# Kernel tuning notes

Hardware: AMD Instinct MI355X
Metric: run time of the kernel (lower is better)

Reference implementation:

```python
import jax, jax.numpy as jnp
import numpy as np

H, W, C = 2160, 3840, 3
K = 1  # kernel_size (splat radius window)


def setup_inputs() -> dict:
    key = jax.random.key(0)
    k1, k2, k3 = jax.random.split(key, 3)
    img = jax.random.normal(k1, (H, W, C), dtype=jnp.float32)
    flow = jax.random.normal(k2, (1, H, W, 2), dtype=jnp.float32) * 4.0  # dx, dy
    depth = jax.random.uniform(k3, (H, W), dtype=jnp.float32, minval=0.1, maxval=10.0)
    return {"img": img, "flow": flow, "depth": depth}


def reference(img, flow, depth):
    """Forward flow-based splatting with per-pixel depth z-buffer test.

    Each source pixel (y,x) is splatted to round((x,y) + flow) within a
    K x K kernel window; where multiple sources land on the same target
    pixel, the one with the smallest depth wins (z-buffer).
    """
    h, w, c = img.shape
    f = flow[0]  # [h, w, 2]
    xs = jnp.arange(w, dtype=f.dtype)
    ys = jnp.arange(h, dtype=f.dtype)
    tx0 = xs[None, :] + f[..., 0]  # target x, [h, w]
    ty0 = ys[:, None] + f[..., 1]  # target y, [h, w]

    offs = [(dy, dx)
            for dy in range(-(K // 2), (K - 1) // 2 + 1)
            for dx in range(-(K // 2), (K - 1) // 2 + 1)]

    dflat = depth.reshape(-1)            # [h*w]
    img_flat = img.reshape(-1, c)        # [h*w, c]

    idx_list, dep_list, src_list = [], [], []
    for dy, dx in offs:
        tx = jnp.round(tx0 + dx).astype(jnp.int32)
        ty = jnp.round(ty0 + dy).astype(jnp.int32)
        valid = (tx >= 0) & (tx < w) & (ty >= 0) & (ty < h)
        lin = jnp.where(valid, ty * w + tx, -1).reshape(-1)  # -1 -> dropped
        idx_list.append(lin)
        dep_list.append(dflat)
        src_list.append(img_flat)

    idx = jnp.concatenate(idx_list)   # [n_splats]
    dep = jnp.concatenate(dep_list)   # [n_splats]
    src = jnp.concatenate(src_list)   # [n_splats, c]

    # Pass 1: scatter-min depth into z-buffer (out-of-bounds dropped).
    zbuf = jnp.full(h * w, jnp.inf, dtype=dep.dtype).at[idx].min(dep, mode='drop')
    # Pass 2: only the depth-test winners write their color.
    win = (dep <= zbuf[jnp.clip(idx, 0, h * w - 1)]) & (idx >= 0)
    widx = jnp.where(win, idx, -1)
    out = jnp.zeros((h * w, c), dtype=img.dtype).at[widx].add(
        src * win[:, None].astype(src.dtype), mode='drop')
    return out.reshape(h, w, c)
```

## Files before the change

kernel.cpp:

```cpp
#include <hip/hip_runtime.h>

constexpr int H = 2160, W = 3840;
constexpr int NPIX = H * W;
constexpr int M = 20;
constexpr int TW = 64, TH = 64;
constexpr int TS = TW * TH;
constexpr int WW = TW + 2 * M;
constexpr int TXN = W / TW;
constexpr int TYN = (H + TH - 1) / TH;
constexpr int NTILES = TXN * TYN;
constexpr int BLK = 1024;
constexpr int QROW = WW / 4;
constexpr int RPP = BLK / QROW;
constexpr unsigned long long EMPTY = ~0ULL;
constexpr unsigned FAR_CAP = 65536;
static_assert(WW % 4 == 0 && RPP * 3 >= TH + 2 * M, "sweep geometry");



__global__ void __launch_bounds__(256)
prep_kernel(const float4* __restrict__ flow4, const float4* __restrict__ depth4,
            uint4* __restrict__ tgt16_4,
            unsigned long long* __restrict__ overlay,
            unsigned int* __restrict__ farcount,
            unsigned int* __restrict__ dirty,
            uint4* __restrict__ farlist)
{
    int tid8 = blockIdx.x * 256 + threadIdx.x;
    unsigned long long oobkey = EMPTY;
    if (tid8 < NPIX / 8) {
        int i0 = tid8 * 8;
        int y  = i0 / W;
        int x0 = i0 - y * W;
        int q0 = tid8 * 2;
        float4 fa0 = flow4[q0 * 2];
        float4 fa1 = flow4[q0 * 2 + 1];
        float4 fb0 = flow4[q0 * 2 + 2];
        float4 fb1 = flow4[q0 * 2 + 3];
        float4 d0  = depth4[q0];
        float4 d1  = depth4[q0 + 1];
        float fx[8] = {fa0.x, fa0.z, fa1.x, fa1.z, fb0.x, fb0.z, fb1.x, fb1.z};
        float fy[8] = {fa0.y, fa0.w, fa1.y, fa1.w, fb0.y, fb0.w, fb1.y, fb1.w};
        float dz[8] = {d0.x, d0.y, d0.z, d0.w, d1.x, d1.y, d1.z, d1.w};
        unsigned short tv[8];
        #pragma unroll
        for (int c = 0; c < 8; ++c) {
            int x = x0 + c;
            int tx = (int)rintf((float)x + fx[c]);
            int ty = (int)rintf((float)y + fy[c]);
            bool valid = ((unsigned)tx < (unsigned)W) && ((unsigned)ty < (unsigned)H);
            unsigned short t = 0xFFFFu;
            if (!valid) {
                unsigned db = __float_as_uint(dz[c]);
                unsigned long long k =
                    ((unsigned long long)db << 32) | 0x80000000u | (unsigned)(i0 + c);
                oobkey = k < oobkey ? k : oobkey;
                dirty[NTILES - 1] = 1;
            } else {
                int dx = tx - x, dy = ty - y;
                bool far = ((unsigned)(dx + M) > (unsigned)(2 * M)) ||
                           ((unsigned)(dy + M) > (unsigned)(2 * M));
                if (far) {
                    unsigned db  = __float_as_uint(dz[c]);
                    int lin = ty * W + tx;
                    unsigned long long key =
                        ((unsigned long long)db << 32) | (unsigned)(i0 + c);
                    atomicMin(&overlay[lin], key);
                    dirty[(ty / TH) * TXN + (tx / TW)] = 1;
                    unsigned slot = atomicAdd(farcount, 1u);
                    if (slot < FAR_CAP)
                        farlist[slot] = make_uint4((unsigned)lin, db,
                                                   (unsigned)(i0 + c), 0u);
                } else {
                    t = (unsigned short)(((dy + M) << 6) | (dx + M));
                }
            }
            tv[c] = t;
        }
        uint4 sv;
        sv.x = (unsigned)tv[0] | ((unsigned)tv[1] << 16);
        sv.y = (unsigned)tv[2] | ((unsigned)tv[3] << 16);
        sv.z = (unsigned)tv[4] | ((unsigned)tv[5] << 16);
        sv.w = (unsigned)tv[6] | ((unsigned)tv[7] << 16);
        tgt16_4[tid8] = sv;
    }
    #pragma unroll
    for (int o = 32; o > 0; o >>= 1) {
        unsigned long long other = __shfl_down(oobkey, o);
        oobkey = other < oobkey ? other : oobkey;
    }
    if ((threadIdx.x & 63) == 0 && oobkey != EMPTY)
        atomicMin(&overlay[NPIX - 1], oobkey);
}

__global__ void __launch_bounds__(BLK, 8)
resolve_kernel(const unsigned short* __restrict__ tgt16,
               const float* __restrict__ depth,
               const float* __restrict__ img,
               unsigned long long* __restrict__ overlay,
               const unsigned int* __restrict__ dirty,
               float* __restrict__ out)
{
    __shared__ unsigned long long lkey[TS];
    __shared__ int lflag;
    const int tid = threadIdx.x;
    const int tile = (blockIdx.x % 8) * (NTILES / 8) + blockIdx.x / 8;
    const int tyi = tile / TXN, txi = tile - tyi * TXN;
    const int ty0 = tyi * TH, tx0 = txi * TW;

    #pragma unroll
    for (int pp = 0; pp < TS / BLK; ++pp) lkey[pp * BLK + tid] = EMPTY;
    if (tid == 0) lflag = 0;
    __syncthreads();

    const int wy_lo = max(ty0 - M, 0);
    const int wy_hi = min(ty0 + TH + M, H);
    const int nrows = wy_hi - wy_lo;
    const int nwin  = nrows * WW;
    const int myrow = tid / QROW;
    const int myq   = tid - myrow * QROW;
    const int gxb   = tx0 - M + myq * 4;
    const bool qok  = (myrow < RPP) && ((unsigned)gxb < (unsigned)W);

    auto LOADR = [&](int pass, ushort4& t4, float4& d4) -> bool {
        int row = pass * RPP + myrow;
        bool act = qok && (row < nrows);
        int gy  = wy_lo + min(row, nrows - 1);
        int gxc = min(max(gxb, 0), W - 4);
        size_t base = (size_t)gy * W + gxc;
        t4 = *(const ushort4*)(&tgt16[base]);
        d4 = *(const float4*)(&depth[base]);
        return act;
    };
    auto PROCR = [&](int pass, bool act, ushort4 t4, float4 d4) {
        if (!act) return;
        int gy = wy_lo + pass * RPP + myrow;
        unsigned tt[4] = {t4.x, t4.y, t4.z, t4.w};
        float    dz[4] = {d4.x, d4.y, d4.z, d4.w};
        #pragma unroll
        for (int c = 0; c < 4; ++c) {
            unsigned t = tt[c];
            int gx = gxb + c;
            int tx = gx + (int)(t & 63u) - M;
            int ty = gy + (int)(t >> 6) - M;
            unsigned ltx = (unsigned)(tx - tx0);
            unsigned lty = (unsigned)(ty - ty0);
            if (ltx >= (unsigned)TW || lty >= (unsigned)TH) continue;
            unsigned p  = lty * TW + ltx;
            unsigned gi = (unsigned)(gy * W + gx);
            unsigned long long key =
                ((unsigned long long)__float_as_uint(dz[c]) << 32) | gi;
            unsigned long long old = atomicMin(&lkey[p], key);
            if ((unsigned)(old >> 32) == (unsigned)(key >> 32) && old != key)
                lflag = 1;
        }
    };

    ushort4 ta, tb; float4 da, db_;
    bool actA = LOADR(0, ta, da);
    bool actB = LOADR(1, tb, db_);
    PROCR(0, actA, ta, da);
    bool actC = LOADR(2, ta, da);
    PROCR(1, actB, tb, db_);
    PROCR(2, actC, ta, da);
    __syncthreads();

    const bool isdirty = dirty[tile] != 0;

    #pragma unroll
    for (int pp = 0; pp < TS / BLK; ++pp) {
        int p = pp * BLK + tid;
        int ly = p >> 6, lx = p & 63;
        int gy = ty0 + ly, gx = tx0 + lx;
        if (gy >= H) continue;
        int gi = gy * W + gx;
        unsigned long long k = lkey[p];
        if (isdirty) {
            unsigned long long o = overlay[gi];
            if ((o >> 32) == (k >> 32) && o != k && k != EMPTY) lflag = 1;
            if (o < k) k = o;
            lkey[p] = k;
            overlay[gi] = k;
        }
        float r = 0.f, g = 0.f, b = 0.f;
        if (k != EMPTY && !((unsigned)k & 0x80000000u)) {
            int src = (int)((unsigned)k & 0x7FFFFFFFu);
            r = img[3 * src + 0];
            g = img[3 * src + 1];
            b = img[3 * src + 2];
        }
        out[3 * gi + 0] = r;
        out[3 * gi + 1] = g;
        out[3 * gi + 2] = b;
    }
    __syncthreads();

    if (lflag) {
        const int wx_lo = tx0 - M;
        for (int j = tid; j < nwin; j += BLK) {
            int wy = j / WW;
            int wx = j - wy * WW;
            int gy = wy_lo + wy;
            int gx = wx_lo + wx;
            if ((unsigned)gx >= (unsigned)W) continue;
            int gi = gy * W + gx;
            unsigned t = tgt16[gi];
            int tx = gx + (int)(t & 63u) - M;
            int ty = gy + (int)(t >> 6) - M;
            unsigned ltx = (unsigned)(tx - tx0);
            unsigned lty = (unsigned)(ty - ty0);
            if (ltx >= (unsigned)TW || lty >= (unsigned)TH) continue;
            unsigned long long k = lkey[lty * TW + ltx];
            unsigned db = __float_as_uint(depth[gi]);
            if ((unsigned)(k >> 32) == db && ((unsigned)k & 0x7FFFFFFFu) != (unsigned)gi) {
                int lin = ty * W + tx;
                atomicAdd(&out[3 * lin + 0], img[3 * gi + 0]);
                atomicAdd(&out[3 * lin + 1], img[3 * gi + 1]);
                atomicAdd(&out[3 * lin + 2], img[3 * gi + 2]);
            }
        }
    }
}

__global__ void __launch_bounds__(256)
farfix_kernel(const uint4* __restrict__ farlist,
              const unsigned int* __restrict__ farcount,
              const unsigned long long* __restrict__ overlay,
              const float* __restrict__ img, float* __restrict__ out)
{
    unsigned n = *farcount;
    if (n > FAR_CAP) n = FAR_CAP;
    for (unsigned r = blockIdx.x * 256 + threadIdx.x; r < n; r += gridDim.x * 256) {
        uint4 rec = farlist[r];
        unsigned long long k = overlay[rec.x];
        if ((unsigned)(k >> 32) == rec.y && ((unsigned)k & 0x7FFFFFFFu) != rec.z) {
            atomicAdd(&out[3 * rec.x + 0], img[3 * rec.z + 0]);
            atomicAdd(&out[3 * rec.x + 1], img[3 * rec.z + 1]);
            atomicAdd(&out[3 * rec.x + 2], img[3 * rec.z + 2]);
        }
    }
}


__global__ void __launch_bounds__(256)
fb_zmin(const float2* __restrict__ flow, const float* __restrict__ depth,
        unsigned long long* __restrict__ zbuf)
{
    int i = blockIdx.x * 256 + threadIdx.x;
    if (i >= NPIX) return;
    int y = i / W, x = i - y * W;
    float2 f = flow[i];
    int tx = (int)rintf((float)x + f.x);
    int ty = (int)rintf((float)y + f.y);
    bool valid = (tx >= 0) && (tx < W) && (ty >= 0) && (ty < H);
    int lin = valid ? (ty * W + tx) : (NPIX - 1);
    unsigned db = __float_as_uint(depth[i]);
    unsigned long long key = ((unsigned long long)db << 32) | (unsigned)i | (valid ? 0u : 0x80000000u);
    if (zbuf[lin] > key) atomicMin(&zbuf[lin], key);
}

__global__ void __launch_bounds__(256)
fb_gather(const unsigned long long* __restrict__ zbuf,
          const float* __restrict__ img, float* __restrict__ out)
{
    int t = blockIdx.x * 256 + threadIdx.x;
    if (t >= NPIX) return;
    unsigned long long key = zbuf[t];
    float r = 0.f, g = 0.f, b = 0.f;
    if (key != EMPTY && !((unsigned)key & 0x80000000u)) {
        int src = (int)((unsigned)key & 0x7FFFFFFFu);
        r = img[3 * src + 0]; g = img[3 * src + 1]; b = img[3 * src + 2];
    }
    out[3 * t + 0] = r; out[3 * t + 1] = g; out[3 * t + 2] = b;
}

__global__ void __launch_bounds__(256)
fb_tiefix(const float2* __restrict__ flow, const float* __restrict__ depth,
          const float* __restrict__ img,
          const unsigned long long* __restrict__ zbuf, float* __restrict__ out)
{
    int i = blockIdx.x * 256 + threadIdx.x;
    if (i >= NPIX) return;
    int y = i / W, x = i - y * W;
    float2 f = flow[i];
    int tx = (int)rintf((float)x + f.x);
    int ty = (int)rintf((float)y + f.y);
    if (tx < 0 || tx >= W || ty < 0 || ty >= H) return;
    int lin = ty * W + tx;
    unsigned long long key = zbuf[lin];
    unsigned db = __float_as_uint(depth[i]);
    if (db == (unsigned)(key >> 32) && (unsigned)key != (unsigned)i) {
        atomicAdd(&out[3 * lin + 0], img[3 * i + 0]);
        atomicAdd(&out[3 * lin + 1], img[3 * i + 1]);
        atomicAdd(&out[3 * lin + 2], img[3 * i + 2]);
    }
}

extern "C" void kernel_launch(void* const* d_in, const int* in_sizes, int n_in,
                              void* d_out, int out_size, void* d_ws, size_t ws_size,
                              hipStream_t stream) {
    const float*  img   = (const float*)d_in[0];
    const float2* flow  = (const float2*)d_in[1];
    const float*  depth = (const float*)d_in[2];
    float* out = (float*)d_out;
    char* ws = (char*)d_ws;

    const size_t off_overlay = (size_t)NPIX * 2;
    const size_t off_meta    = off_overlay + (size_t)NPIX * 8;
    const size_t off_dirty   = off_meta + 16;
    const size_t off_far     = off_dirty + (size_t)NTILES * 4;
    const size_t need = off_far + (size_t)FAR_CAP * 16;

    dim3 blk(256), grd((NPIX + 255) / 256);

    if (ws_size >= need) {
        uint4*              tgt16_4  = (uint4*)ws;
        unsigned long long* overlay  = (unsigned long long*)(ws + off_overlay);
        unsigned int*       farcount = (unsigned int*)(ws + off_meta);
        unsigned int*       dirtyf   = (unsigned int*)(ws + off_dirty);
        uint4*              farlist  = (uint4*)(ws + off_far);

        hipMemsetAsync(ws + off_meta, 0, 16 + (size_t)NTILES * 4, stream);

        prep_kernel<<<dim3(NPIX / 8 / 256), blk, 0, stream>>>(
            (const float4*)flow, (const float4*)depth, tgt16_4, overlay,
            farcount, dirtyf, farlist);
        resolve_kernel<<<dim3(NTILES), dim3(BLK), 0, stream>>>(
            (const unsigned short*)ws, depth, img, overlay, dirtyf, out);
        farfix_kernel<<<dim3(64), blk, 0, stream>>>(farlist, farcount, overlay,
                                                    img, out);
    } else {
        unsigned long long* zbuf = (unsigned long long*)ws;
        hipMemsetAsync(zbuf, 0xFF, (size_t)NPIX * 8, stream);
        fb_zmin  <<<grd, blk, 0, stream>>>(flow, depth, zbuf);
        fb_gather<<<grd, blk, 0, stream>>>(zbuf, img, out);
        fb_tiefix<<<grd, blk, 0, stream>>>(flow, depth, img, zbuf, out);
    }
}
```

Measured before the change: 111.9 us.

## Fuse far-splat fixup into resolve kernel, shrink tiles, add nontemporal accesses

Removes the separate farfix kernel launch and instead has each dirty tile scan the far list and apply tie fixups for its own pixels using the shared-memory key buffer. Tiles are halved to 64x32 with 512-thread blocks and a fourth row pass. The shared-memory init now runs after the first loads are issued, the overlay writeback is dropped, and flow loads and output stores are made nontemporal. The risk is that every dirty tile rescans the whole far list, which is redundant work when that list is large, and the smaller tiles add halo overhead.

```diff
diff --git a/kernel.cpp b/kernel.cpp
--- a/kernel.cpp
+++ b/kernel.cpp
@@ -3,23 +3,25 @@
 constexpr int H = 2160, W = 3840;
 constexpr int NPIX = H * W;
 constexpr int M = 20;
-constexpr int TW = 64, TH = 64;
+constexpr int TW = 64, TH = 32;
 constexpr int TS = TW * TH;
 constexpr int WW = TW + 2 * M;
 constexpr int TXN = W / TW;
 constexpr int TYN = (H + TH - 1) / TH;
 constexpr int NTILES = TXN * TYN;
-constexpr int BLK = 1024;
+constexpr int BLK = 512;
 constexpr int QROW = WW / 4;
 constexpr int RPP = BLK / QROW;
 constexpr unsigned long long EMPTY = ~0ULL;
 constexpr unsigned FAR_CAP = 65536;
-static_assert(WW % 4 == 0 && RPP * 3 >= TH + 2 * M, "sweep geometry");
+static_assert(WW % 4 == 0 && RPP * 4 >= TH + 2 * M, "sweep geometry");
+
+typedef float f32x4 __attribute__((ext_vector_type(4)));
 
 
 
 __global__ void __launch_bounds__(256)
-prep_kernel(const float4* __restrict__ flow4, const float4* __restrict__ depth4,
+prep_kernel(const f32x4* __restrict__ flow4, const float4* __restrict__ depth4,
             uint4* __restrict__ tgt16_4,
             unsigned long long* __restrict__ overlay,
             unsigned int* __restrict__ farcount,
@@ -33,12 +35,12 @@
         int y  = i0 / W;
         int x0 = i0 - y * W;
         int q0 = tid8 * 2;
-        float4 fa0 = flow4[q0 * 2];
-        float4 fa1 = flow4[q0 * 2 + 1];
-        float4 fb0 = flow4[q0 * 2 + 2];
-        float4 fb1 = flow4[q0 * 2 + 3];
-        float4 d0  = depth4[q0];
-        float4 d1  = depth4[q0 + 1];
+        f32x4 fa0 = __builtin_nontemporal_load(&flow4[q0 * 2]);
+        f32x4 fa1 = __builtin_nontemporal_load(&flow4[q0 * 2 + 1]);
+        f32x4 fb0 = __builtin_nontemporal_load(&flow4[q0 * 2 + 2]);
+        f32x4 fb1 = __builtin_nontemporal_load(&flow4[q0 * 2 + 3]);
+        float4 d0 = depth4[q0];
+        float4 d1 = depth4[q0 + 1];
         float fx[8] = {fa0.x, fa0.z, fa1.x, fa1.z, fb0.x, fb0.z, fb1.x, fb1.z};
         float fy[8] = {fa0.y, fa0.w, fa1.y, fa1.w, fb0.y, fb0.w, fb1.y, fb1.w};
         float dz[8] = {d0.x, d0.y, d0.z, d0.w, d1.x, d1.y, d1.z, d1.w};
@@ -97,8 +99,10 @@
 resolve_kernel(const unsigned short* __restrict__ tgt16,
                const float* __restrict__ depth,
                const float* __restrict__ img,
-               unsigned long long* __restrict__ overlay,
+               const unsigned long long* __restrict__ overlay,
                const unsigned int* __restrict__ dirty,
+               const unsigned int* __restrict__ farcount,
+               const uint4* __restrict__ farlist,
                float* __restrict__ out)
 {
     __shared__ unsigned long long lkey[TS];
@@ -107,11 +111,7 @@
     const int tile = (blockIdx.x % 8) * (NTILES / 8) + blockIdx.x / 8;
     const int tyi = tile / TXN, txi = tile - tyi * TXN;
     const int ty0 = tyi * TH, tx0 = txi * TW;
-
-    #pragma unroll
-    for (int pp = 0; pp < TS / BLK; ++pp) lkey[pp * BLK + tid] = EMPTY;
-    if (tid == 0) lflag = 0;
-    __syncthreads();
+    const bool isdirty = dirty[tile] != 0;
 
     const int wy_lo = max(ty0 - M, 0);
     const int wy_hi = min(ty0 + TH + M, H);
@@ -159,13 +159,19 @@
     ushort4 ta, tb; float4 da, db_;
     bool actA = LOADR(0, ta, da);
     bool actB = LOADR(1, tb, db_);
+
+    #pragma unroll
+    for (int pp = 0; pp < TS / BLK; ++pp) lkey[pp * BLK + tid] = EMPTY;
+    if (tid == 0) lflag = 0;
+    __syncthreads();
+
     PROCR(0, actA, ta, da);
     bool actC = LOADR(2, ta, da);
     PROCR(1, actB, tb, db_);
+    bool actD = LOADR(3, tb, db_);
     PROCR(2, actC, ta, da);
+    PROCR(3, actD, tb, db_);
     __syncthreads();
-
-    const bool isdirty = dirty[tile] != 0;
 
     #pragma unroll
     for (int pp = 0; pp < TS / BLK; ++pp) {
@@ -178,9 +184,7 @@
         if (isdirty) {
             unsigned long long o = overlay[gi];
             if ((o >> 32) == (k >> 32) && o != k && k != EMPTY) lflag = 1;
-            if (o < k) k = o;
-            lkey[p] = k;
-            overlay[gi] = k;
+            if (o < k) { k = o; lkey[p] = k; }
         }
         float r = 0.f, g = 0.f, b = 0.f;
         if (k != EMPTY && !((unsigned)k & 0x80000000u)) {
@@ -189,11 +193,29 @@
             g = img[3 * src + 1];
             b = img[3 * src + 2];
         }
-        out[3 * gi + 0] = r;
-        out[3 * gi + 1] = g;
-        out[3 * gi + 2] = b;
+        __builtin_nontemporal_store(r, &out[3 * gi + 0]);
+        __builtin_nontemporal_store(g, &out[3 * gi + 1]);
+        __builtin_nontemporal_store(b, &out[3 * gi + 2]);
     }
     __syncthreads();
+
+    if (isdirty) {
+        unsigned n = *farcount;
+        if (n > FAR_CAP) n = FAR_CAP;
+        for (unsigned r = tid; r < n; r += BLK) {
+            uint4 rec = farlist[r];
+            unsigned ty = rec.x / (unsigned)W;
+            unsigned tx = rec.x - ty * (unsigned)W;
+            if ((int)(ty / TH) != tyi || (int)(tx / TW) != txi) continue;
+            unsigned p = (ty - (unsigned)ty0) * TW + (tx - (unsigned)tx0);
+            unsigned long long k = lkey[p];
+            if ((unsigned)(k >> 32) == rec.y && ((unsigned)k & 0x7FFFFFFFu) != rec.z) {
+                atomicAdd(&out[3 * rec.x + 0], img[3 * rec.z + 0]);
+                atomicAdd(&out[3 * rec.x + 1], img[3 * rec.z + 1]);
+                atomicAdd(&out[3 * rec.x + 2], img[3 * rec.z + 2]);
+            }
+        }
+    }
 
     if (lflag) {
         const int wx_lo = tx0 - M;
@@ -222,25 +244,6 @@
     }
 }
 
-__global__ void __launch_bounds__(256)
-farfix_kernel(const uint4* __restrict__ farlist,
-              const unsigned int* __restrict__ farcount,
-              const unsigned long long* __restrict__ overlay,
-              const float* __restrict__ img, float* __restrict__ out)
-{
-    unsigned n = *farcount;
-    if (n > FAR_CAP) n = FAR_CAP;
-    for (unsigned r = blockIdx.x * 256 + threadIdx.x; r < n; r += gridDim.x * 256) {
-        uint4 rec = farlist[r];
-        unsigned long long k = overlay[rec.x];
-        if ((unsigned)(k >> 32) == rec.y && ((unsigned)k & 0x7FFFFFFFu) != rec.z) {
-            atomicAdd(&out[3 * rec.x + 0], img[3 * rec.z + 0]);
-            atomicAdd(&out[3 * rec.x + 1], img[3 * rec.z + 1]);
-            atomicAdd(&out[3 * rec.x + 2], img[3 * rec.z + 2]);
-        }
-    }
-}
-
 
 __global__ void __launch_bounds__(256)
 fb_zmin(const float2* __restrict__ flow, const float* __restrict__ depth,
@@ -323,12 +326,11 @@
         hipMemsetAsync(ws + off_meta, 0, 16 + (size_t)NTILES * 4, stream);
 
         prep_kernel<<<dim3(NPIX / 8 / 256), blk, 0, stream>>>(
-            (const float4*)flow, (const float4*)depth, tgt16_4, overlay,
+            (const f32x4*)flow, (const float4*)depth, tgt16_4, overlay,
             farcount, dirtyf, farlist);
         resolve_kernel<<<dim3(NTILES), dim3(BLK), 0, stream>>>(
-            (const unsigned short*)ws, depth, img, overlay, dirtyf, out);
-        farfix_kernel<<<dim3(64), blk, 0, stream>>>(farlist, farcount, overlay,
-                                                    img, out);
+            (const unsigned short*)ws, depth, img, overlay, dirtyf,
+            farcount, farlist, out);
     } else {
         unsigned long long* zbuf = (unsigned long long*)ws;
         hipMemsetAsync(zbuf, 0xFF, (size_t)NPIX * 8, stream);
```

Measured after the change: 91.89 us, median of 2. 17.9% less time.
